# Kernel optimization log

Hardware: AMD Instinct MI355X
Metric: run time of the kernel (lower is better)

The kernel has to match this reference:

```python
import jax, jax.numpy as jnp
import numpy as np

P = 5        # window_size
HEADS = 8
DH = 32      # dim_head
SCALE = DH ** -0.5


def setup_inputs() -> dict:
    key = jax.random.key(0)
    ks = jax.random.split(key, 5)
    b, c, h = 32, 256, 4000
    inner = HEADS * DH  # 256
    x = jax.random.normal(ks[0], (b, c, h), dtype=jnp.float32)
    W_qkv = jax.random.normal(ks[1], (c, inner * 3), dtype=jnp.float32) * (c ** -0.5)
    W_out = jax.random.normal(ks[2], (inner, c), dtype=jnp.float32) * (inner ** -0.5)
    b_out = jax.random.normal(ks[3], (c,), dtype=jnp.float32) * 0.02
    pos_embedding = jax.random.normal(ks[4], (2 * P - 1, 2 * P - 1), dtype=jnp.float32) * 0.02
    return {"x": x, "W_qkv": W_qkv, "W_out": W_out, "b_out": b_out, "pos_embedding": pos_embedding}


def _local_attn(x, W_qkv, W_out, b_out, pos_embedding):
    b, c, h = x.shape
    n = h // P
    # relative-position bias, faithful to torch indexing: rel_index[:,0]=(p-1-a), rel_index[:,1]=(p-a), shape (p,1)
    a = jnp.arange(P)
    bias = pos_embedding[(P - 1 - a)[:, None], (P - a)[:, None]]  # (p, 1)
    mask = jnp.zeros((P, P), x.dtype) + bias                      # (p, p)
    # 'b c (n p) -> (b n) p c'
    xw = x.reshape(b, c, n, P).transpose(0, 2, 3, 1).reshape(b * n, P, c)
    qkv = xw @ W_qkv  # (B, p, 3*inner)
    q, k, v = jnp.split(qkv, 3, axis=-1)
    split_heads = lambda t: t.reshape(b * n, P, HEADS, DH).transpose(0, 2, 1, 3)  # (B, h, p, d)
    q, k, v = split_heads(q), split_heads(k), split_heads(v)
    dots = jnp.einsum('bhid,bhjd->bhij', q, k) * SCALE + mask
    attn = jax.nn.softmax(dots, axis=-1)
    out = jnp.einsum('bhij,bhjd->bhid', attn, v)            # (B, h, p, d)
    out = out.transpose(0, 2, 1, 3).reshape(b * n, P, HEADS * DH)
    out = out @ W_out + b_out                                # (B, p, c_out)
    # '(b n) p c -> b c (n p)'
    out = out.reshape(b, n, P, -1).transpose(0, 3, 1, 2).reshape(b, -1, n * P)
    return out, attn


def reference(x, W_qkv, W_out, b_out, pos_embedding):
    return _local_attn(x, W_qkv, W_out, b_out, pos_embedding)
```

## Files before the change

kernel.cpp:

```cpp
#include <hip/hip_runtime.h>
#include <hip/hip_bf16.h>

typedef __attribute__((ext_vector_type(8))) short short8;
typedef __attribute__((ext_vector_type(4))) float f32x4;

namespace {
constexpr int kC = 256;
constexpr int kH = 4000;
constexpr int kNW = 800;
constexpr int kP = 5;
constexpr int kHeads = 8;
constexpr float kScale = 0.17677669529663687f;
constexpr int kTotalWin = 32 * kNW;

constexpr int WPB = 6;
constexpr int ROWS = WPB * kP;
constexpr int MT = 2;
constexpr int NTHR = 512;

constexpr int WQKV_PACKED = 3 * 16 * 8 * 64 * 8;
constexpr int WOUT_PACKED = 16 * 8 * 64 * 8;

constexpr int RK = 15360;
constexpr int RV = 30720;
constexpr int SM_TOTAL = 46080;
}

__device__ inline float b2f(short s) {
  union { unsigned u; float f; } v;
  v.u = ((unsigned)(unsigned short)s) << 16;
  return v.f;
}
__device__ inline unsigned short f2bs(float f) {
  __hip_bfloat16 h = __float2bfloat16(f);
  return *reinterpret_cast<unsigned short*>(&h);
}

__global__ void prep_weights(const float* __restrict__ Wqkv,
                             const float* __restrict__ Wout,
                             __hip_bfloat16* __restrict__ wq_p,
                             __hip_bfloat16* __restrict__ wo_p) {
  int idx = blockIdx.x * 256 + threadIdx.x;
  if (idx < WQKV_PACKED) {
    int i = idx & 7;
    int l = (idx >> 3) & 63;
    int kt = (idx >> 9) & 7;
    int nt = (idx >> 12) & 15;
    int part = idx >> 16;
    int k = kt * 32 + (l >> 4) * 8 + i;
    int col = part * 256 + nt * 16 + (l & 15);
    wq_p[idx] = __float2bfloat16(Wqkv[k * 768 + col]);
  }
  if (idx < WOUT_PACKED) {
    int i = idx & 7;
    int l = (idx >> 3) & 63;
    int kt = (idx >> 9) & 7;
    int nt = (idx >> 12) & 15;
    int k = kt * 32 + (l >> 4) * 8 + i;
    int col = nt * 16 + (l & 15);
    wo_p[idx] = __float2bfloat16(Wout[k * 256 + col]);
  }
}

__global__ __launch_bounds__(NTHR, 3) void local_attn_kernel(
    const float* __restrict__ x, const short* __restrict__ wq_p,
    const short* __restrict__ wo_p, const float* __restrict__ b_out,
    float* __restrict__ g_out, float* __restrict__ g_attn) {
  __shared__ __align__(16) char smem[SM_TOTAL];

  const int tid = threadIdx.x;
  const int lane = tid & 63;
  const int wid = tid >> 6;

  const int widx0 = blockIdx.x * WPB;
  const int nwin = min(WPB, kTotalWin - widx0);
  const int nrows = nwin * kP;

  for (int i = tid; i < (kC / 2) * ROWS; i += NTHR) {
    int cp = i / ROWS, hh = i % ROWS;
    if (hh < nrows) {
      int gw = widx0 + hh / kP;
      int b = gw / kNW;
      int hl = (gw - b * kNW) * kP + hh % kP;
      const float* p = x + ((size_t)b * kC + 2 * cp) * kH + hl;
      unsigned u = (unsigned)f2bs(p[0]) | ((unsigned)f2bs(p[kH]) << 16);
      *(unsigned*)(smem + hh * 512 + ((cp * 4) ^ ((hh & 7) << 4))) = u;
    }
  }
  __syncthreads();

  for (int pi = 0; pi < 2; ++pi) {
    const int part = pi + 1;
    f32x4 acc[MT][2];
#pragma unroll
    for (int m = 0; m < MT; ++m)
#pragma unroll
      for (int n = 0; n < 2; ++n) acc[m][n] = (f32x4){0.f, 0.f, 0.f, 0.f};
#pragma unroll
    for (int kt = 0; kt < 8; ++kt) {
      short8 a[MT];
#pragma unroll
      for (int m = 0; m < MT; ++m) {
        int row = m * 16 + (lane & 15);
        int kb = kt * 64 + ((lane >> 4) << 4);
        a[m] = *(const short8*)(smem + row * 512 + (kb ^ ((row & 7) << 4)));
      }
      short8 b[2];
#pragma unroll
      for (int n = 0; n < 2; ++n) {
        int nt = wid * 2 + n;
        b[n] = *(const short8*)(wq_p +
                                ((((part * 16 + nt) * 8 + kt) * 64 + lane) * 8));
      }
#pragma unroll
      for (int m = 0; m < MT; ++m)
#pragma unroll
        for (int n = 0; n < 2; ++n)
          acc[m][n] = __builtin_amdgcn_mfma_f32_16x16x32_bf16(a[m], b[n],
                                                              acc[m][n], 0, 0, 0);
    }
    char* dst = smem + part * RK;
#pragma unroll
    for (int m = 0; m < MT; ++m)
#pragma unroll
      for (int n = 0; n < 2; ++n)
#pragma unroll
        for (int r = 0; r < 4; ++r) {
          int row = m * 16 + ((lane >> 4) << 2) + r;
          if (row < ROWS) {
            int col = wid * 32 + n * 16 + (lane & 15);
            *(__hip_bfloat16*)(dst + row * 512 + ((col * 2) ^ ((row & 7) << 4))) =
                __float2bfloat16(acc[m][n][r]);
          }
        }
  }
  {
    f32x4 accq[MT][2];
#pragma unroll
    for (int m = 0; m < MT; ++m)
#pragma unroll
      for (int n = 0; n < 2; ++n) accq[m][n] = (f32x4){0.f, 0.f, 0.f, 0.f};
#pragma unroll
    for (int kt = 0; kt < 8; ++kt) {
      short8 a[MT];
#pragma unroll
      for (int m = 0; m < MT; ++m) {
        int row = m * 16 + (lane & 15);
        int kb = kt * 64 + ((lane >> 4) << 4);
        a[m] = *(const short8*)(smem + row * 512 + (kb ^ ((row & 7) << 4)));
      }
      short8 b[2];
#pragma unroll
      for (int n = 0; n < 2; ++n) {
        int nt = wid * 2 + n;
        b[n] = *(const short8*)(wq_p + (((nt * 8 + kt) * 64 + lane) * 8));
      }
#pragma unroll
      for (int m = 0; m < MT; ++m)
#pragma unroll
        for (int n = 0; n < 2; ++n)
          accq[m][n] = __builtin_amdgcn_mfma_f32_16x16x32_bf16(a[m], b[n],
                                                               accq[m][n], 0, 0, 0);
    }
    __syncthreads();
#pragma unroll
    for (int m = 0; m < MT; ++m)
#pragma unroll
      for (int n = 0; n < 2; ++n)
#pragma unroll
        for (int r = 0; r < 4; ++r) {
          int row = m * 16 + ((lane >> 4) << 2) + r;
          if (row < ROWS) {
            int col = wid * 32 + n * 16 + (lane & 15);
            *(__hip_bfloat16*)(smem + row * 512 + ((col * 2) ^ ((row & 7) << 4))) =
                __float2bfloat16(accq[m][n][r]);
          }
        }
  }
  __syncthreads();

  const int task = tid >> 1, half = tid & 1;
  const bool act = task < nwin * (kHeads * kP);
  float p5[kP];
  int qrow = 0, head = 0, wl = 0, cbase = 0, qsw = 0;
  if (act) {
    wl = task / (kHeads * kP);
    int rem = task % (kHeads * kP);
    head = rem / kP;
    int i = rem % kP;
    qrow = wl * kP + i;
    qsw = (qrow & 7) << 4;
    cbase = head * 64 + half * 32;

    float qf[16];
#pragma unroll
    for (int ch = 0; ch < 2; ++ch) {
      short8 v8 = *(const short8*)(smem + qrow * 512 + ((cbase + ch * 16) ^ qsw));
#pragma unroll
      for (int e = 0; e < 8; ++e) qf[ch * 8 + e] = b2f(v8[e]);
    }
    float mx = -1e30f;
#pragma unroll
    for (int j = 0; j < kP; ++j) {
      int krow = wl * kP + j;
      int ksw = (krow & 7) << 4;
      float s = 0.f;
#pragma unroll
      for (int ch = 0; ch < 2; ++ch) {
        short8 kv =
            *(const short8*)(smem + RK + krow * 512 + ((cbase + ch * 16) ^ ksw));
#pragma unroll
        for (int e = 0; e < 8; ++e) s += qf[ch * 8 + e] * b2f(kv[e]);
      }
      s += __shfl_xor(s, 1);
      s *= kScale;
      p5[j] = s;
      mx = fmaxf(mx, s);
    }
    float sum = 0.f;
#pragma unroll
    for (int j = 0; j < kP; ++j) {
      p5[j] = __expf(p5[j] - mx);
      sum += p5[j];
    }
    float inv = 1.f / sum;
#pragma unroll
    for (int j = 0; j < kP; ++j) p5[j] *= inv;
    if (!half) {
      float* ap = g_attn + (size_t)(widx0 + wl) * 200 + head * 25 + i * 5;
#pragma unroll
      for (int j = 0; j < kP; ++j) ap[j] = p5[j];
    }
  }
  __syncthreads();

  if (act) {
    float ov[16];
#pragma unroll
    for (int d = 0; d < 16; ++d) ov[d] = 0.f;
#pragma unroll
    for (int j = 0; j < kP; ++j) {
      float aj = p5[j];
      int vrow = wl * kP + j;
      int vsw = (vrow & 7) << 4;
#pragma unroll
      for (int ch = 0; ch < 2; ++ch) {
        short8 vv =
            *(const short8*)(smem + RV + vrow * 512 + ((cbase + ch * 16) ^ vsw));
#pragma unroll
        for (int e = 0; e < 8; ++e) ov[ch * 8 + e] += aj * b2f(vv[e]);
      }
    }
#pragma unroll
    for (int ch = 0; ch < 2; ++ch) {
      short8 o8;
#pragma unroll
      for (int e = 0; e < 8; ++e) o8[e] = (short)f2bs(ov[ch * 8 + e]);
      *(short8*)(smem + qrow * 512 + ((cbase + ch * 16) ^ qsw)) = o8;
    }
  }
  __syncthreads();

  f32x4 acc2[MT][2];
#pragma unroll
  for (int m = 0; m < MT; ++m)
#pragma unroll
    for (int n = 0; n < 2; ++n) acc2[m][n] = (f32x4){0.f, 0.f, 0.f, 0.f};
#pragma unroll
  for (int kt = 0; kt < 8; ++kt) {
    short8 a[MT];
#pragma unroll
    for (int m = 0; m < MT; ++m) {
      int row = m * 16 + (lane & 15);
      int kb = kt * 64 + ((lane >> 4) << 4);
      a[m] = *(const short8*)(smem + row * 512 + (kb ^ ((row & 7) << 4)));
    }
    short8 b[2];
#pragma unroll
    for (int n = 0; n < 2; ++n) {
      int nt = wid * 2 + n;
      b[n] = *(const short8*)(wo_p + (((nt * 8 + kt) * 64 + lane) * 8));
    }
#pragma unroll
    for (int m = 0; m < MT; ++m)
#pragma unroll
      for (int n = 0; n < 2; ++n)
        acc2[m][n] = __builtin_amdgcn_mfma_f32_16x16x32_bf16(a[m], b[n],
                                                             acc2[m][n], 0, 0, 0);
  }
  float* outS = (float*)(smem + RK);
#pragma unroll
  for (int n = 0; n < 2; ++n) {
    int col = wid * 32 + n * 16 + (lane & 15);
    float bias = b_out[col];
#pragma unroll
    for (int m = 0; m < MT; ++m)
#pragma unroll
      for (int r = 0; r < 4; ++r) {
        int row = m * 16 + ((lane >> 4) << 2) + r;
        if (row < ROWS) outS[col * ROWS + row] = acc2[m][n][r] + bias;
      }
  }
  __syncthreads();

  for (int i = tid; i < kC * ROWS; i += NTHR) {
    int c = i / ROWS, hh = i % ROWS;
    if (hh < nrows) {
      int gw = widx0 + hh / kP;
      int b = gw / kNW;
      int hl = (gw - b * kNW) * kP + hh % kP;
      g_out[((size_t)b * kC + c) * kH + hl] = outS[c * ROWS + hh];
    }
  }
}

extern "C" void kernel_launch(void* const* d_in, const int* in_sizes, int n_in,
                              void* d_out, int out_size, void* d_ws,
                              size_t ws_size, hipStream_t stream) {
  const float* x = (const float*)d_in[0];
  const float* Wqkv = (const float*)d_in[1];
  const float* Wout = (const float*)d_in[2];
  const float* bout = (const float*)d_in[3];

  short* wq_p = (short*)d_ws;
  short* wo_p = wq_p + WQKV_PACKED;

  prep_weights<<<WQKV_PACKED / 256, 256, 0, stream>>>(
      Wqkv, Wout, (__hip_bfloat16*)wq_p, (__hip_bfloat16*)wo_p);

  float* g_out = (float*)d_out;
  float* g_attn = g_out + (size_t)32 * kC * kH;

  int nblocks = (kTotalWin + WPB - 1) / WPB;
  local_attn_kernel<<<nblocks, NTHR, 0, stream>>>(x, wq_p, wo_p, bout, g_out,
                                                  g_attn);
}
```

Baseline: 199.4 us.

## Compute per-window attention scores and PV product with MFMA instead of scalar loops

Replaces the scalar per-thread QK dot products and attention-weighted V sums with block-level MFMA tiles. Each wave handles one head: it computes a 32x32 QK^T tile, stores only the diagonal-window scores to LDS, and runs the softmax in 240 threads. The probabilities are then written into a zero-padded bf16 tile and multiplied against a transposed, swizzled V layout with MFMA. This removes most per-thread bf16 unpacking and FMA work, at the cost of computing mostly-masked 32x32 products, extra LDS layouts and barriers, and rounding probabilities to bf16 before the PV step.

New measurement: 191.5 us. 1.04x faster.

```diff
diff --git a/kernel.cpp b/kernel.cpp
--- a/kernel.cpp
+++ b/kernel.cpp
@@ -9,9 +9,8 @@
 constexpr int kH = 4000;
 constexpr int kNW = 800;
 constexpr int kP = 5;
-constexpr int kHeads = 8;
 constexpr float kScale = 0.17677669529663687f;
-constexpr int kTotalWin = 32 * kNW;
+constexpr int kTotalWin = 25600;
 
 constexpr int WPB = 6;
 constexpr int ROWS = WPB * kP;
@@ -21,9 +20,9 @@
 constexpr int WQKV_PACKED = 3 * 16 * 8 * 64 * 8;
 constexpr int WOUT_PACKED = 16 * 8 * 64 * 8;
 
-constexpr int RK = 15360;
-constexpr int RV = 30720;
-constexpr int SM_TOTAL = 46080;
+constexpr int RKOFF = 15360;
+constexpr int RVT = 30720;
+constexpr int SM_TOTAL = 47104;
 }
 
 __device__ inline float b2f(short s) {
@@ -87,6 +86,11 @@
       *(unsigned*)(smem + hh * 512 + ((cp * 4) ^ ((hh & 7) << 4))) = u;
     }
   }
+  if (tid < 256) {
+    int h = tid >> 5, d = tid & 31;
+    int phys = 3 ^ ((d >> 1) & 3);
+    *(unsigned*)(smem + RVT + h * 2048 + d * 64 + phys * 16 + 12) = 0u;
+  }
   __syncthreads();
 
   for (int pi = 0; pi < 2; ++pi) {
@@ -119,20 +123,38 @@
           acc[m][n] = __builtin_amdgcn_mfma_f32_16x16x32_bf16(a[m], b[n],
                                                               acc[m][n], 0, 0, 0);
     }
-    char* dst = smem + part * RK;
-#pragma unroll
-    for (int m = 0; m < MT; ++m)
-#pragma unroll
-      for (int n = 0; n < 2; ++n)
-#pragma unroll
-        for (int r = 0; r < 4; ++r) {
-          int row = m * 16 + ((lane >> 4) << 2) + r;
-          if (row < ROWS) {
-            int col = wid * 32 + n * 16 + (lane & 15);
-            *(__hip_bfloat16*)(dst + row * 512 + ((col * 2) ^ ((row & 7) << 4))) =
-                __float2bfloat16(acc[m][n][r]);
+    if (part == 1) {
+#pragma unroll
+      for (int m = 0; m < MT; ++m)
+#pragma unroll
+        for (int n = 0; n < 2; ++n)
+#pragma unroll
+          for (int r = 0; r < 4; ++r) {
+            int row = m * 16 + ((lane >> 4) << 2) + r;
+            if (row < ROWS) {
+              int col = wid * 32 + n * 16 + (lane & 15);
+              *(__hip_bfloat16*)(smem + RKOFF + row * 512 +
+                                 ((col * 2) ^ ((row & 7) << 4))) =
+                  __float2bfloat16(acc[m][n][r]);
+            }
           }
-        }
+    } else {
+#pragma unroll
+      for (int m = 0; m < MT; ++m)
+#pragma unroll
+        for (int n = 0; n < 2; ++n)
+#pragma unroll
+          for (int r = 0; r < 4; ++r) {
+            int ks = m * 16 + ((lane >> 4) << 2) + r;
+            if (ks < ROWS) {
+              int d = n * 16 + (lane & 15);
+              int lb = ks * 2;
+              int phys = (lb >> 4) ^ ((d >> 1) & 3);
+              *(__hip_bfloat16*)(smem + RVT + wid * 2048 + d * 64 + phys * 16 +
+                                 (lb & 15)) = __float2bfloat16(acc[m][n][r]);
+            }
+          }
+    }
   }
   {
     f32x4 accq[MT][2];
@@ -179,85 +201,118 @@
   }
   __syncthreads();
 
-  const int task = tid >> 1, half = tid & 1;
-  const bool act = task < nwin * (kHeads * kP);
-  float p5[kP];
-  int qrow = 0, head = 0, wl = 0, cbase = 0, qsw = 0;
-  if (act) {
-    wl = task / (kHeads * kP);
-    int rem = task % (kHeads * kP);
-    head = rem / kP;
-    int i = rem % kP;
-    qrow = wl * kP + i;
-    qsw = (qrow & 7) << 4;
-    cbase = head * 64 + half * 32;
-
-    float qf[16];
-#pragma unroll
-    for (int ch = 0; ch < 2; ++ch) {
-      short8 v8 = *(const short8*)(smem + qrow * 512 + ((cbase + ch * 16) ^ qsw));
-#pragma unroll
-      for (int e = 0; e < 8; ++e) qf[ch * 8 + e] = b2f(v8[e]);
-    }
-    float mx = -1e30f;
-#pragma unroll
-    for (int j = 0; j < kP; ++j) {
-      int krow = wl * kP + j;
-      int ksw = (krow & 7) << 4;
-      float s = 0.f;
-#pragma unroll
-      for (int ch = 0; ch < 2; ++ch) {
-        short8 kv =
-            *(const short8*)(smem + RK + krow * 512 + ((cbase + ch * 16) ^ ksw));
-#pragma unroll
-        for (int e = 0; e < 8; ++e) s += qf[ch * 8 + e] * b2f(kv[e]);
-      }
-      s += __shfl_xor(s, 1);
-      s *= kScale;
-      p5[j] = s;
-      mx = fmaxf(mx, s);
-    }
-    float sum = 0.f;
-#pragma unroll
-    for (int j = 0; j < kP; ++j) {
-      p5[j] = __expf(p5[j] - mx);
-      sum += p5[j];
-    }
-    float inv = 1.f / sum;
-#pragma unroll
-    for (int j = 0; j < kP; ++j) p5[j] *= inv;
-    if (!half) {
-      float* ap = g_attn + (size_t)(widx0 + wl) * 200 + head * 25 + i * 5;
-#pragma unroll
-      for (int j = 0; j < kP; ++j) ap[j] = p5[j];
-    }
-  }
-  __syncthreads();
-
-  if (act) {
-    float ov[16];
-#pragma unroll
-    for (int d = 0; d < 16; ++d) ov[d] = 0.f;
-#pragma unroll
-    for (int j = 0; j < kP; ++j) {
-      float aj = p5[j];
-      int vrow = wl * kP + j;
-      int vsw = (vrow & 7) << 4;
-#pragma unroll
-      for (int ch = 0; ch < 2; ++ch) {
-        short8 vv =
-            *(const short8*)(smem + RV + vrow * 512 + ((cbase + ch * 16) ^ vsw));
-#pragma unroll
-        for (int e = 0; e < 8; ++e) ov[ch * 8 + e] += aj * b2f(vv[e]);
-      }
-    }
-#pragma unroll
-    for (int ch = 0; ch < 2; ++ch) {
-      short8 o8;
-#pragma unroll
-      for (int e = 0; e < 8; ++e) o8[e] = (short)f2bs(ov[ch * 8 + e]);
-      *(short8*)(smem + qrow * 512 + ((cbase + ch * 16) ^ qsw)) = o8;
-    }
+  f32x4 sacc[2][2];
+  {
+    short8 qa[2], kb2[2];
+#pragma unroll
+    for (int mt = 0; mt < 2; ++mt) {
+      int row = mt * 16 + (lane & 15);
+      qa[mt] = *(const short8*)(smem + row * 512 +
+                                ((wid * 64 + ((lane >> 4) << 4)) ^ ((row & 7) << 4)));
+    }
+#pragma unroll
+    for (int nt = 0; nt < 2; ++nt) {
+      int row = nt * 16 + (lane & 15);
+      kb2[nt] = *(const short8*)(smem + RKOFF + row * 512 +
+                                 ((wid * 64 + ((lane >> 4) << 4)) ^ ((row & 7) << 4)));
+    }
+#pragma unroll
+    for (int mt = 0; mt < 2; ++mt)
+#pragma unroll
+      for (int nt = 0; nt < 2; ++nt)
+        sacc[mt][nt] = __builtin_amdgcn_mfma_f32_16x16x32_bf16(
+            qa[mt], kb2[nt], (f32x4){0.f, 0.f, 0.f, 0.f}, 0, 0, 0);
+  }
+  __syncthreads();
+
+#pragma unroll
+  for (int mt = 0; mt < 2; ++mt)
+#pragma unroll
+    for (int nt = 0; nt < 2; ++nt)
+#pragma unroll
+      for (int r = 0; r < 4; ++r) {
+        int qrow = mt * 16 + ((lane >> 4) << 2) + r;
+        int krow = nt * 16 + (lane & 15);
+        int qw = qrow / 5, kw = krow / 5;
+        if (qrow < ROWS && krow < ROWS && qw == kw) {
+          int jj = (krow - kw * 5) * 4;
+          int phys = (((jj >> 4) ^ ((qrow >> 1) & 3)) << 4) | (jj & 15);
+          *(float*)(smem + RKOFF + wid * 1920 + qrow * 64 + phys) =
+              sacc[mt][nt][r] * kScale;
+        }
+      }
+  __syncthreads();
+
+  if (tid < 240) {
+    int q = tid % 30, h = tid / 30;
+    int w = q / 5, i = q - w * 5;
+    if (w < nwin) {
+      char* base = smem + RKOFF + h * 1920 + q * 64;
+      int csw = (q >> 1) & 3;
+      float p[5], mx = -1e30f;
+#pragma unroll
+      for (int j = 0; j < 5; ++j) {
+        int jj = j * 4;
+        p[j] = *(const float*)(base + ((((jj >> 4) ^ csw) << 4) | (jj & 15)));
+        mx = fmaxf(mx, p[j]);
+      }
+      float sum = 0.f;
+#pragma unroll
+      for (int j = 0; j < 5; ++j) {
+        p[j] = __expf(p[j] - mx);
+        sum += p[j];
+      }
+      float inv = 1.f / sum;
+      float* ap = g_attn + (size_t)(widx0 + w) * 200 + h * 25 + i * 5;
+#pragma unroll
+      for (int j = 0; j < 5; ++j) {
+        p[j] *= inv;
+        ap[j] = p[j];
+      }
+      short8 z = (short8){0, 0, 0, 0, 0, 0, 0, 0};
+#pragma unroll
+      for (int c = 0; c < 4; ++c) *(short8*)(base + c * 16) = z;
+#pragma unroll
+      for (int j = 0; j < 5; ++j) {
+        int lb = (w * 5 + j) * 2;
+        *(unsigned short*)(base + ((((lb >> 4) ^ csw) << 4) | (lb & 15))) =
+            f2bs(p[j]);
+      }
+    }
+  }
+  __syncthreads();
+
+  {
+    short8 va[2], pb[2];
+#pragma unroll
+    for (int mt = 0; mt < 2; ++mt) {
+      int d = mt * 16 + (lane & 15);
+      int phys = ((lane >> 4) ^ ((d >> 1) & 3)) << 4;
+      va[mt] = *(const short8*)(smem + RVT + wid * 2048 + d * 64 + phys);
+    }
+#pragma unroll
+    for (int nt = 0; nt < 2; ++nt) {
+      int q = nt * 16 + (lane & 15);
+      int phys = ((lane >> 4) ^ ((q >> 1) & 3)) << 4;
+      pb[nt] = *(const short8*)(smem + RKOFF + wid * 1920 + q * 64 + phys);
+    }
+#pragma unroll
+    for (int mt = 0; mt < 2; ++mt)
+#pragma unroll
+      for (int nt = 0; nt < 2; ++nt) {
+        f32x4 o = __builtin_amdgcn_mfma_f32_16x16x32_bf16(
+            va[mt], pb[nt], (f32x4){0.f, 0.f, 0.f, 0.f}, 0, 0, 0);
+#pragma unroll
+        for (int r = 0; r < 4; ++r) {
+          int d = mt * 16 + ((lane >> 4) << 2) + r;
+          int q = nt * 16 + (lane & 15);
+          if (q < ROWS) {
+            int cb = wid * 64 + d * 2;
+            *(__hip_bfloat16*)(smem + q * 512 + (cb ^ ((q & 7) << 4))) =
+                __float2bfloat16(o[r]);
+          }
+        }
+      }
   }
   __syncthreads();
 
@@ -288,7 +343,7 @@
         acc2[m][n] = __builtin_amdgcn_mfma_f32_16x16x32_bf16(a[m], b[n],
                                                              acc2[m][n], 0, 0, 0);
   }
-  float* outS = (float*)(smem + RK);
+  float* outS = (float*)(smem + RKOFF);
 #pragma unroll
   for (int n = 0; n < 2; ++n) {
     int col = wid * 32 + n * 16 + (lane & 15);
```
